# Optimization experiments

Measured on AMD Instinct MI355X. Metric: run time of the kernel, lower is better.

Reference implementation:

```python
import jax, jax.numpy as jnp
import numpy as np

T, B, OBS, H, P, L, A = 512, 128, 512, 256, 128, 4, 4


def _ln(x, scale, bias, eps=1e-6):
    mu = jnp.mean(x, axis=-1, keepdims=True)
    var = jnp.mean((x - mu) ** 2, axis=-1, keepdims=True)
    return (x - mu) * jax.lax.rsqrt(var + eps) * scale + bias


def _binop(qi, qj):
    # S5 reset-aware associative operator: elements (A, b, reset_flag)
    Ai, bi, ci = qi
    Aj, bj, cj = qj
    A = (Aj * Ai) * (1.0 - cj) + Aj * cj
    b = (Aj * bi + bj) * (1.0 - cj) + bj * cj
    c = ci * (1.0 - cj) + cj
    return A, b, c


def _s5_layer(x, dones, h0, scale, bias, lam_re, lam_im, b_re, b_im, c_re, c_im, d_vec, log_step, glu_W, glu_b):
    # x: (T,B,H) real, dones: (T,B), h0: (B,P) complex64
    skip = x
    u = _ln(x, scale, bias)                                  # prenorm
    lam = lam_re + 1j * lam_im                               # (P,)
    step = jnp.exp(log_step)                                 # (P,)
    lam_bar = jnp.exp(lam * step)                            # ZOH discretization
    B_bar = ((lam_bar - 1.0) / lam)[:, None] * (b_re + 1j * b_im)  # (P,H)
    Bu = jnp.einsum('tbh,ph->tbp', u.astype(jnp.complex64), B_bar)  # (T,B,P)
    A_el = jnp.concatenate([jnp.ones((1, B, P), jnp.complex64),
                            jnp.broadcast_to(lam_bar.astype(jnp.complex64), (T, B, P))], axis=0)
    b_el = jnp.concatenate([h0[None], Bu], axis=0)
    c_el = jnp.concatenate([jnp.zeros((1, B, 1), jnp.float32), dones[..., None]], axis=0)
    _, xs, _ = jax.lax.associative_scan(_binop, (A_el, b_el, c_el), axis=0)
    xs = xs[1:]                                              # (T,B,P) complex states
    new_h = xs[-1]
    C = c_re + 1j * c_im                                     # (H,P)
    ys = 2.0 * jnp.real(jnp.einsum('tbp,hp->tbh', xs, C)) + d_vec * u  # conj_sym output + D*u
    z = _ln(ys, scale, bias)                                 # gtrxl norm (shared LayerNorm params)
    z = jax.nn.gelu(z)                                       # half_glu1
    z = z * jax.nn.sigmoid(z @ glu_W + glu_b)
    return skip + z, new_h


def setup_inputs() -> dict:
    key = jax.random.key(0)
    ks = jax.random.split(key, 40)
    f32 = jnp.float32

    def n(i, shape, s=1.0):
        return jax.random.normal(ks[i], shape, f32) * s

    inp = {}
    inp['obs'] = n(0, (T, B, OBS))
    inp['dones'] = (jax.random.uniform(ks[1], (T, B)) < 0.01).astype(f32)
    inp['hidden_re'] = jnp.zeros((L, B, P), f32)
    inp['hidden_im'] = jnp.zeros((L, B, P), f32)
    inp['enc0_W'] = n(2, (OBS, 128), 1.0 / np.sqrt(OBS))
    inp['enc0_b'] = jnp.zeros((128,), f32)
    inp['enc1_W'] = n(3, (128, H), 1.0 / np.sqrt(128))
    inp['enc1_b'] = jnp.zeros((H,), f32)
    inp['norm_scale'] = jnp.ones((L, H), f32)
    inp['norm_bias'] = jnp.zeros((L, H), f32)
    inp['Lambda_re'] = -0.5 * jax.random.uniform(ks[4], (L, P), f32) - 0.1
    inp['Lambda_im'] = n(5, (L, P), np.pi)
    inp['B_re'] = n(6, (L, P, H), 1.0 / np.sqrt(H))
    inp['B_im'] = n(7, (L, P, H), 1.0 / np.sqrt(H))
    inp['C_re'] = n(8, (L, H, P), 1.0 / np.sqrt(2 * P))
    inp['C_im'] = n(9, (L, H, P), 1.0 / np.sqrt(2 * P))
    inp['D'] = n(10, (L, H))
    inp['log_step'] = jax.random.uniform(ks[11], (L, P), f32, np.log(1e-3), np.log(1e-1))
    inp['glu_W'] = n(12, (L, H, H), 1.0 / np.sqrt(H))
    inp['glu_b'] = jnp.zeros((L, H), f32)
    inp['ab0_W'] = n(13, (H, 128), 1.0 / np.sqrt(H))
    inp['ab0_b'] = jnp.zeros((128,), f32)
    inp['ab1_W'] = n(14, (128, 128), 1.0 / np.sqrt(128))
    inp['ab1_b'] = jnp.zeros((128,), f32)
    inp['adec_W'] = n(15, (128, A), 0.01 / np.sqrt(128))
    inp['adec_b'] = jnp.full((A,), 0.5, f32)
    inp['log_std'] = jnp.full((A,), -0.7, f32)
    inp['vb0_W'] = n(16, (H, 128), 1.0 / np.sqrt(H))
    inp['vb0_b'] = jnp.zeros((128,), f32)
    inp['vb1_W'] = n(17, (128, 128), 1.0 / np.sqrt(128))
    inp['vb1_b'] = jnp.zeros((128,), f32)
    inp['vdec_W'] = n(18, (128, 1), 1.0 / np.sqrt(128))
    inp['vdec_b'] = jnp.zeros((1,), f32)
    return inp


def reference(obs, dones, hidden_re, hidden_im, enc0_W, enc0_b, enc1_W, enc1_b,
              norm_scale, norm_bias, Lambda_re, Lambda_im, B_re, B_im, C_re, C_im,
              D, log_step, glu_W, glu_b, ab0_W, ab0_b, ab1_W, ab1_b, adec_W, adec_b,
              log_std, vb0_W, vb0_b, vb1_W, vb1_b, vdec_W, vdec_b):
    e = jax.nn.leaky_relu(obs @ enc0_W + enc0_b)
    e = jax.nn.leaky_relu(e @ enc1_W + enc1_b)
    h0 = (hidden_re + 1j * hidden_im).astype(jnp.complex64)  # (L,B,P)
    new_h = []
    for l in range(L):
        e, hl = _s5_layer(e, dones, h0[l], norm_scale[l], norm_bias[l],
                          Lambda_re[l], Lambda_im[l], B_re[l], B_im[l],
                          C_re[l], C_im[l], D[l], log_step[l], glu_W[l], glu_b[l])
        new_h.append(hl)
    new_h = jnp.stack(new_h)
    am = jax.nn.leaky_relu(e @ ab0_W + ab0_b)
    am = jax.nn.leaky_relu(am @ ab1_W + ab1_b)
    am = am @ adec_W + adec_b                                # actor mean (T,B,A)
    v = jax.nn.leaky_relu(e @ vb0_W + vb0_b)
    v = jax.nn.leaky_relu(v @ vb1_W + vb1_b)
    v = v @ vdec_W + vdec_b                                  # critic (T,B,1)
    sc = jnp.broadcast_to(jnp.exp(log_std), am.shape)        # Normal scale (pi params)
    out = jnp.concatenate([am, sc, v], axis=-1)              # (T,B,2A+1)
    return out, jnp.real(new_h), jnp.imag(new_h)
```

## Files before the change

kernel.cpp:

```cpp
#include <hip/hip_runtime.h>
#include <math.h>

#define TT 512
#define BB 128
#define OBSD 512
#define HD 256
#define PD 128
#define LD 4
#define NTB (TT*BB)

typedef __bf16 bf16x8 __attribute__((ext_vector_type(8)));
typedef float  f32x4  __attribute__((ext_vector_type(4)));

__device__ __forceinline__ float bf2f(unsigned short u) {
    return __uint_as_float(((unsigned)u) << 16);
}
__device__ __forceinline__ unsigned short f2bf(float f) {
    unsigned u = __float_as_uint(f);
    unsigned r = (u + 0x7FFFu + ((u >> 16) & 1u)) >> 16;
    return (unsigned short)r;
}
__device__ __forceinline__ float gelu_f(float x) {
    float x3 = x * x * x;
    return 0.5f * x * (1.f + tanhf(0.7978845608028654f * (x + 0.044715f * x3)));
}

template<int MODE, int NJ>
__global__ __launch_bounds__(256) void mgemm2(
    const unsigned short* __restrict__ A, const unsigned short* __restrict__ BT,
    int K, const float* __restrict__ bias,
    const float* __restrict__ lnsc, const float* __restrict__ lnbi,
    const unsigned short* __restrict__ aux1, unsigned short* Xio,
    unsigned short* __restrict__ U, int wU)
{
    const int N = NJ * 64;
    __shared__ unsigned short smA[64 * 32];
    __shared__ unsigned short smB[NJ * 64 * 32];
    __shared__ float2 red[64][4];
    int tid = threadIdx.x;
    int lane = tid & 63, w = tid >> 6;
    int m16 = lane & 15, quad = lane >> 4;
    int m0 = blockIdx.x * 64;

    f32x4 acc[4][NJ] = {};

    for (int k0 = 0; k0 < K; k0 += 32) {
        {
            const unsigned short* g = A + (size_t)(m0 + (tid >> 2)) * K + k0 + (tid & 3) * 8;
            unsigned short* l = smA + tid * 8;
            __builtin_amdgcn_global_load_lds(
                (const __attribute__((address_space(1))) void*)g,
                (__attribute__((address_space(3))) void*)l, 16, 0, 0);
        }
#pragma unroll
        for (int p = 0; p < NJ; ++p) {
            const unsigned short* g = BT + (size_t)(p * 64 + (tid >> 2)) * K + k0 + (tid & 3) * 8;
            unsigned short* l = smB + p * 2048 + tid * 8;
            __builtin_amdgcn_global_load_lds(
                (const __attribute__((address_space(1))) void*)g,
                (__attribute__((address_space(3))) void*)l, 16, 0, 0);
        }
        __syncthreads();
        bf16x8 af[4], bfr[NJ];
#pragma unroll
        for (int mi = 0; mi < 4; ++mi)
            af[mi] = *(const bf16x8*)(smA + (mi * 16 + m16) * 32 + quad * 8);
#pragma unroll
        for (int nj = 0; nj < NJ; ++nj)
            bfr[nj] = *(const bf16x8*)(smB + (w * NJ * 16 + nj * 16 + m16) * 32 + quad * 8);
#pragma unroll
        for (int mi = 0; mi < 4; ++mi)
#pragma unroll
            for (int nj = 0; nj < NJ; ++nj)
                acc[mi][nj] = __builtin_amdgcn_mfma_f32_16x16x32_bf16(
                    bfr[nj], af[mi], acc[mi][nj], 0, 0, 0);
        __syncthreads();
    }

    int colb = w * NJ * 16 + quad * 4;

    if (MODE == 1) {
#pragma unroll
        for (int mi = 0; mi < 4; ++mi) {
            size_t rowb = (size_t)(m0 + mi * 16 + m16) * N;
#pragma unroll
            for (int nj = 0; nj < NJ; ++nj) {
                ushort4 o = { f2bf(acc[mi][nj][0]), f2bf(acc[mi][nj][1]),
                              f2bf(acc[mi][nj][2]), f2bf(acc[mi][nj][3]) };
                *(ushort4*)(U + rowb + colb + nj * 16) = o;
            }
        }
        return;
    }

    float4 bn[NJ];
#pragma unroll
    for (int nj = 0; nj < NJ; ++nj) bn[nj] = *(const float4*)(bias + colb + nj * 16);

#pragma unroll
    for (int mi = 0; mi < 4; ++mi) {
        size_t rowb = (size_t)(m0 + mi * 16 + m16) * N;
        float s = 0.f, q = 0.f;
#pragma unroll
        for (int nj = 0; nj < NJ; ++nj) {
            ushort4 a1, xo;
            if (MODE == 2 || MODE == 3) a1 = *(const ushort4*)(aux1 + rowb + colb + nj * 16);
            if (MODE == 3)              xo = *(const ushort4*)(Xio + rowb + colb + nj * 16);
            float vv[4];
#pragma unroll
            for (int r = 0; r < 4; ++r) {
                float v = acc[mi][nj][r];
                float bv = (r == 0) ? bn[nj].x : (r == 1) ? bn[nj].y : (r == 2) ? bn[nj].z : bn[nj].w;
                if (MODE == 0 || MODE == 4) {
                    v += bv; v = v > 0.f ? v : 0.01f * v;
                } else if (MODE == 2) {
                    float u = bf2f(r == 0 ? a1.x : r == 1 ? a1.y : r == 2 ? a1.z : a1.w);
                    v += bv * u;
                } else if (MODE == 3) {
                    float zz = bf2f(r == 0 ? a1.x : r == 1 ? a1.y : r == 2 ? a1.z : a1.w);
                    float xx = bf2f(r == 0 ? xo.x : r == 1 ? xo.y : r == 2 ? xo.z : xo.w);
                    float sg = 1.f / (1.f + expf(-(v + bv)));
                    v = xx + zz * sg;
                }
                vv[r] = v;
                acc[mi][nj][r] = v;
                s += v; q += v * v;
            }
            if (MODE == 0 || MODE == 3) {
                ushort4 o = { f2bf(vv[0]), f2bf(vv[1]), f2bf(vv[2]), f2bf(vv[3]) };
                *(ushort4*)(Xio + rowb + colb + nj * 16) = o;
            } else if (MODE == 4) {
                ushort4 o = { f2bf(vv[0]), f2bf(vv[1]), f2bf(vv[2]), f2bf(vv[3]) };
                *(ushort4*)(U + rowb + colb + nj * 16) = o;
            }
        }
        if (MODE != 4 && (MODE != 3 || wU)) {
            s += __shfl_xor(s, 16); q += __shfl_xor(q, 16);
            s += __shfl_xor(s, 32); q += __shfl_xor(q, 32);
            if (quad == 0) red[mi * 16 + m16][w] = float2{s, q};
        }
    }
    if (MODE == 4 || (MODE == 3 && !wU)) return;
    __syncthreads();

    float4 ls[NJ], lb[NJ];
#pragma unroll
    for (int nj = 0; nj < NJ; ++nj) {
        ls[nj] = *(const float4*)(lnsc + colb + nj * 16);
        lb[nj] = *(const float4*)(lnbi + colb + nj * 16);
    }
#pragma unroll
    for (int mi = 0; mi < 4; ++mi) {
        int row_l = mi * 16 + m16;
        float2 t0 = red[row_l][0], t1 = red[row_l][1], t2 = red[row_l][2], t3 = red[row_l][3];
        float S = t0.x + t1.x + t2.x + t3.x;
        float Q = t0.y + t1.y + t2.y + t3.y;
        float mu = S * (1.f / 256.f);
        float var = Q * (1.f / 256.f) - mu * mu;
        float rstd = rsqrtf(var + 1e-6f);
        size_t rowb = (size_t)(m0 + row_l) * N;
#pragma unroll
        for (int nj = 0; nj < NJ; ++nj) {
            float o[4];
#pragma unroll
            for (int r = 0; r < 4; ++r) {
                float sc = (r == 0) ? ls[nj].x : (r == 1) ? ls[nj].y : (r == 2) ? ls[nj].z : ls[nj].w;
                float bi = (r == 0) ? lb[nj].x : (r == 1) ? lb[nj].y : (r == 2) ? lb[nj].z : lb[nj].w;
                float v = (acc[mi][nj][r] - mu) * rstd * sc + bi;
                if (MODE == 2) v = gelu_f(v);
                o[r] = v;
            }
            ushort4 ov = { f2bf(o[0]), f2bf(o[1]), f2bf(o[2]), f2bf(o[3]) };
            *(ushort4*)(U + rowb + colb + nj * 16) = ov;
        }
    }
}

__global__ __launch_bounds__(256) void mgemm_obs(
    const float* __restrict__ A, const unsigned short* __restrict__ BT,
    unsigned short* __restrict__ U, const float* __restrict__ bias)
{
    const int K = 512, NJ = 2, N = 128;
    __shared__ unsigned short smA[64 * 32];
    __shared__ unsigned short smB[NJ * 64 * 32];
    int tid = threadIdx.x;
    int lane = tid & 63, w = tid >> 6;
    int m16 = lane & 15, quad = lane >> 4;
    int m0 = blockIdx.x * 64;

    f32x4 acc[4][NJ] = {};
    for (int k0 = 0; k0 < K; k0 += 32) {
#pragma unroll
        for (int p = 0; p < 2; ++p) {
            int idx = p * 256 + tid;
            int r = idx >> 3, kq = (idx & 7) * 4;
            float4 v = *(const float4*)(A + (size_t)(m0 + r) * K + k0 + kq);
            ushort4 o = { f2bf(v.x), f2bf(v.y), f2bf(v.z), f2bf(v.w) };
            *(ushort4*)(smA + r * 32 + kq) = o;
        }
#pragma unroll
        for (int p = 0; p < NJ; ++p) {
            const unsigned short* g = BT + (size_t)(p * 64 + (tid >> 2)) * K + k0 + (tid & 3) * 8;
            unsigned short* l = smB + p * 2048 + tid * 8;
            __builtin_amdgcn_global_load_lds(
                (const __attribute__((address_space(1))) void*)g,
                (__attribute__((address_space(3))) void*)l, 16, 0, 0);
        }
        __syncthreads();
        bf16x8 af[4], bfr[NJ];
#pragma unroll
        for (int mi = 0; mi < 4; ++mi)
            af[mi] = *(const bf16x8*)(smA + (mi * 16 + m16) * 32 + quad * 8);
#pragma unroll
        for (int nj = 0; nj < NJ; ++nj)
            bfr[nj] = *(const bf16x8*)(smB + (w * NJ * 16 + nj * 16 + m16) * 32 + quad * 8);
#pragma unroll
        for (int mi = 0; mi < 4; ++mi)
#pragma unroll
            for (int nj = 0; nj < NJ; ++nj)
                acc[mi][nj] = __builtin_amdgcn_mfma_f32_16x16x32_bf16(
                    bfr[nj], af[mi], acc[mi][nj], 0, 0, 0);
        __syncthreads();
    }
    int colb = w * NJ * 16 + quad * 4;
#pragma unroll
    for (int mi = 0; mi < 4; ++mi) {
        size_t rowb = (size_t)(m0 + mi * 16 + m16) * N;
#pragma unroll
        for (int nj = 0; nj < NJ; ++nj) {
            float4 bv = *(const float4*)(bias + colb + nj * 16);
            float v0 = acc[mi][nj][0] + bv.x; v0 = v0 > 0.f ? v0 : 0.01f * v0;
            float v1 = acc[mi][nj][1] + bv.y; v1 = v1 > 0.f ? v1 : 0.01f * v1;
            float v2 = acc[mi][nj][2] + bv.z; v2 = v2 > 0.f ? v2 : 0.01f * v2;
            float v3 = acc[mi][nj][3] + bv.w; v3 = v3 > 0.f ? v3 : 0.01f * v3;
            ushort4 o = { f2bf(v0), f2bf(v1), f2bf(v2), f2bf(v3) };
            *(ushort4*)(U + rowb + colb + nj * 16) = o;
        }
    }
}

__global__ __launch_bounds__(512) void scan2_k(
    const unsigned short* __restrict__ bu, unsigned short* __restrict__ xs,
    const float* __restrict__ dones,
    const float* __restrict__ h0re, const float* __restrict__ h0im,
    const float* __restrict__ lamre, const float* __restrict__ lamim,
    const float* __restrict__ lstep,
    float* __restrict__ outre, float* __restrict__ outim)
{
    __shared__ float sdone[TT];
    __shared__ float4 ssum[8][64];
    __shared__ float2 shin[8][64];
    int tid = threadIdx.x;
    int b  = blockIdx.x >> 1;
    int ph = blockIdx.x & 1;
    int chunk = tid >> 6, pl = tid & 63;
    int p = ph * 64 + pl;
    sdone[tid] = dones[tid * BB + b];
    float lr = lamre[p], li = lamim[p];
    float st = expf(lstep[p]);
    float er = expf(lr * st);
    float ar = er * cosf(li * st);
    float ai = er * sinf(li * st);
    __syncthreads();

    int t0 = chunk * 64;
    unsigned buf[64];
    float Ar = 1.f, Ai = 0.f, br = 0.f, bi = 0.f;
#pragma unroll
    for (int j = 0; j < 64; ++j) {
        size_t off = ((size_t)(t0 + j) * BB + b) * 256 + 2 * p;
        unsigned v = *(const unsigned*)(bu + off);
        buf[j] = v;
        float bur = bf2f((unsigned short)(v & 0xFFFFu));
        float bui = bf2f((unsigned short)(v >> 16));
        if (sdone[t0 + j] != 0.f) {
            Ar = 0.f; Ai = 0.f; br = bur; bi = bui;
        } else {
            float nAr = ar * Ar - ai * Ai;
            float nAi = ar * Ai + ai * Ar;
            float nbr = fmaf(ar, br, fmaf(-ai, bi, bur));
            float nbi = fmaf(ar, bi, fmaf(ai, br, bui));
            Ar = nAr; Ai = nAi; br = nbr; bi = nbi;
        }
    }
    ssum[chunk][pl] = float4{Ar, Ai, br, bi};
    __syncthreads();
    if (tid < 64) {
        int gid = b * 128 + p;
        float hr = h0re[gid], hi = h0im[gid];
#pragma unroll
        for (int c = 0; c < 8; ++c) {
            shin[c][pl] = float2{hr, hi};
            float4 s = ssum[c][pl];
            float nhr = fmaf(s.x, hr, fmaf(-s.y, hi, s.z));
            float nhi = fmaf(s.x, hi, fmaf(s.y, hr, s.w));
            hr = nhr; hi = nhi;
        }
        outre[gid] = hr; outim[gid] = hi;
    }
    __syncthreads();
    float hr = shin[chunk][pl].x, hi = shin[chunk][pl].y;
#pragma unroll
    for (int j = 0; j < 64; ++j) {
        unsigned v = buf[j];
        float bur = bf2f((unsigned short)(v & 0xFFFFu));
        float bui = bf2f((unsigned short)(v >> 16));
        float nr, ni;
        if (sdone[t0 + j] != 0.f) { nr = bur; ni = bui; }
        else {
            nr = fmaf(ar, hr, fmaf(-ai, hi, bur));
            ni = fmaf(ar, hi, fmaf(ai, hr, bui));
        }
        hr = nr; hi = ni;
        size_t off = ((size_t)(t0 + j) * BB + b) * 256 + 2 * p;
        *(unsigned*)(xs + off) = ((unsigned)f2bf(ni) << 16) | f2bf(nr);
    }
}

__global__ __launch_bounds__(256) void prep_k(
    const float* __restrict__ Br, const float* __restrict__ Bi,
    const float* __restrict__ Cr, const float* __restrict__ Ci,
    const float* __restrict__ Lr, const float* __restrict__ Li,
    const float* __restrict__ ls, unsigned short* bbarT, unsigned short* ccatT)
{
    int gid = blockIdx.x * 256 + threadIdx.x;
    int l = gid >> 15;
    int rem = gid & 32767;
    int p = rem >> 8;
    int h = rem & 255;
    float lr = Lr[l * PD + p], li = Li[l * PD + p];
    float st = expf(ls[l * PD + p]);
    float er = expf(lr * st);
    float lbr = er * cosf(li * st);
    float lbi = er * sinf(li * st);
    float nr = lbr - 1.f, ni = lbi;
    float den = lr * lr + li * li;
    float fr = (nr * lr + ni * li) / den;
    float fi = (ni * lr - nr * li) / den;
    float bre = Br[(size_t)(l * PD + p) * HD + h];
    float bim = Bi[(size_t)(l * PD + p) * HD + h];
    size_t lb = (size_t)l * 65536;
    bbarT[lb + (size_t)(2 * p) * 256 + h]     = f2bf(fr * bre - fi * bim);
    bbarT[lb + (size_t)(2 * p + 1) * 256 + h] = f2bf(fr * bim + fi * bre);
    float cre = Cr[(size_t)(l * HD + h) * PD + p];
    float cim = Ci[(size_t)(l * HD + h) * PD + p];
    ccatT[lb + (size_t)h * 256 + 2 * p]     = f2bf(2.f * cre);
    ccatT[lb + (size_t)h * 256 + 2 * p + 1] = f2bf(-2.f * cim);
}

__global__ __launch_bounds__(256) void tcvt_k(const float* __restrict__ in,
    unsigned short* __restrict__ out, int K, int N)
{
    int gid = blockIdx.x * 256 + threadIdx.x;
    if (gid >= K * N) return;
    int k = gid / N, n = gid - k * N;
    out[(size_t)n * K + k] = f2bf(in[gid]);
}

__global__ __launch_bounds__(256) void head_k(
    const unsigned short* __restrict__ am2, const unsigned short* __restrict__ v2,
    const float* __restrict__ adW, const float* __restrict__ adb,
    const float* __restrict__ lstd,
    const float* __restrict__ vdW, const float* __restrict__ vdb,
    float* out)
{
    int wid = threadIdx.x >> 6, lane = threadIdx.x & 63;
    size_t row = (size_t)blockIdx.x * 4 + wid;
    float a1 = bf2f(am2[row * 128 + lane]);
    float a2 = bf2f(am2[row * 128 + 64 + lane]);
    float w1 = bf2f(v2[row * 128 + lane]);
    float w2 = bf2f(v2[row * 128 + 64 + lane]);
    float vals[5];
#pragma unroll
    for (int a = 0; a < 4; ++a)
        vals[a] = a1 * adW[lane * 4 + a] + a2 * adW[(lane + 64) * 4 + a];
    vals[4] = w1 * vdW[lane] + w2 * vdW[64 + lane];
#pragma unroll
    for (int off = 32; off; off >>= 1)
#pragma unroll
        for (int k = 0; k < 5; ++k) vals[k] += __shfl_xor(vals[k], off);
    if (lane == 0) {
        size_t o = row * 9;
#pragma unroll
        for (int a = 0; a < 4; ++a) out[o + a] = vals[a] + adb[a];
#pragma unroll
        for (int a = 0; a < 4; ++a) out[o + 4 + a] = expf(lstd[a]);
        out[o + 8] = vals[4] + vdb[0];
    }
}

extern "C" void kernel_launch(void* const* d_in, const int* in_sizes, int n_in,
                              void* d_out, int out_size, void* d_ws, size_t ws_size,
                              hipStream_t stream) {
    (void)in_sizes; (void)n_in; (void)out_size; (void)ws_size;
    const float* obs     = (const float*)d_in[0];
    const float* dones   = (const float*)d_in[1];
    const float* hre     = (const float*)d_in[2];
    const float* him     = (const float*)d_in[3];
    const float* enc0_W  = (const float*)d_in[4];
    const float* enc0_b  = (const float*)d_in[5];
    const float* enc1_W  = (const float*)d_in[6];
    const float* enc1_b  = (const float*)d_in[7];
    const float* nsc     = (const float*)d_in[8];
    const float* nbi     = (const float*)d_in[9];
    const float* Lre     = (const float*)d_in[10];
    const float* Lim     = (const float*)d_in[11];
    const float* B_re    = (const float*)d_in[12];
    const float* B_im    = (const float*)d_in[13];
    const float* C_re    = (const float*)d_in[14];
    const float* C_im    = (const float*)d_in[15];
    const float* Dv      = (const float*)d_in[16];
    const float* lstep   = (const float*)d_in[17];
    const float* glu_W   = (const float*)d_in[18];
    const float* glu_b   = (const float*)d_in[19];
    const float* ab0_W   = (const float*)d_in[20];
    const float* ab0_b   = (const float*)d_in[21];
    const float* ab1_W   = (const float*)d_in[22];
    const float* ab1_b   = (const float*)d_in[23];
    const float* adec_W  = (const float*)d_in[24];
    const float* adec_b  = (const float*)d_in[25];
    const float* log_std = (const float*)d_in[26];
    const float* vb0_W   = (const float*)d_in[27];
    const float* vb0_b   = (const float*)d_in[28];
    const float* vb1_W   = (const float*)d_in[29];
    const float* vb1_b   = (const float*)d_in[30];
    const float* vdec_W  = (const float*)d_in[31];
    const float* vdec_b  = (const float*)d_in[32];

    const size_t MB = (size_t)1 << 20;
    char* wsb = (char*)d_ws;
    unsigned short* XS    = (unsigned short*)(wsb);
    unsigned short* AM1   = (unsigned short*)(wsb);
    unsigned short* V1    = (unsigned short*)(wsb + 16 * MB);
    unsigned short* AM2   = (unsigned short*)(wsb + 32 * MB);
    unsigned short* V2    = (unsigned short*)(wsb + 48 * MB);
    unsigned short* U1    = (unsigned short*)(wsb + 64 * MB);
    unsigned short* X     = (unsigned short*)(wsb + 96 * MB);
    unsigned short* U     = (unsigned short*)(wsb + 128 * MB);
    unsigned short* BU    = (unsigned short*)(wsb + 160 * MB);
    char* wgt = wsb + 192 * MB;
    unsigned short* BBART = (unsigned short*)(wgt);
    unsigned short* CCATT = (unsigned short*)(wgt + 512 * 1024);
    unsigned short* GLUT  = (unsigned short*)(wgt + 1024 * 1024);
    unsigned short* E0T   = (unsigned short*)(wgt + 1536 * 1024);
    unsigned short* E1T   = (unsigned short*)(wgt + 1664 * 1024);
    unsigned short* AB0T  = (unsigned short*)(wgt + 1728 * 1024);
    unsigned short* AB1T  = (unsigned short*)(wgt + 1792 * 1024);
    unsigned short* VB0T  = (unsigned short*)(wgt + 1824 * 1024);
    unsigned short* VB1T  = (unsigned short*)(wgt + 1888 * 1024);

    float* out   = (float*)d_out;
    float* outre = out + (size_t)NTB * 9;
    float* outim = outre + LD * BB * PD;

    prep_k<<<512, 256, 0, stream>>>(B_re, B_im, C_re, C_im, Lre, Lim, lstep, BBART, CCATT);
    tcvt_k<<<256, 256, 0, stream>>>(enc0_W, E0T, 512, 128);
    tcvt_k<<<128, 256, 0, stream>>>(enc1_W, E1T, 128, 256);
    for (int l = 0; l < LD; ++l)
        tcvt_k<<<256, 256, 0, stream>>>(glu_W + (size_t)l * 65536, GLUT + (size_t)l * 65536, 256, 256);
    tcvt_k<<<128, 256, 0, stream>>>(ab0_W, AB0T, 256, 128);
    tcvt_k<<<64, 256, 0, stream>>>(ab1_W, AB1T, 128, 128);
    tcvt_k<<<128, 256, 0, stream>>>(vb0_W, VB0T, 256, 128);
    tcvt_k<<<64, 256, 0, stream>>>(vb1_W, VB1T, 128, 128);

    mgemm_obs<<<1024, 256, 0, stream>>>(obs, E0T, U1, enc0_b);
    mgemm2<0, 4><<<1024, 256, 0, stream>>>(U1, E1T, 128, enc1_b, nsc, nbi, nullptr, X, U, 1);

    for (int l = 0; l < LD; ++l) {
        mgemm2<1, 4><<<1024, 256, 0, stream>>>(U, BBART + (size_t)l * 65536, 256,
                                               nullptr, nullptr, nullptr, nullptr, nullptr, BU, 0);
        scan2_k<<<256, 512, 0, stream>>>(BU, XS, dones, hre + l * BB * PD, him + l * BB * PD,
                                         Lre + l * PD, Lim + l * PD, lstep + l * PD,
                                         outre + l * BB * PD, outim + l * BB * PD);
        mgemm2<2, 4><<<1024, 256, 0, stream>>>(XS, CCATT + (size_t)l * 65536, 256,
                                               Dv + l * HD, nsc + l * HD, nbi + l * HD, U, nullptr, U, 1);
        const float* nsc2 = nsc + ((l + 1 < LD) ? (l + 1) * HD : 0);
        const float* nbi2 = nbi + ((l + 1 < LD) ? (l + 1) * HD : 0);
        mgemm2<3, 4><<<1024, 256, 0, stream>>>(U, GLUT + (size_t)l * 65536, 256,
                                               glu_b + l * HD, nsc2, nbi2, U, X, U, (l + 1 < LD) ? 1 : 0);
    }

    mgemm2<4, 2><<<1024, 256, 0, stream>>>(X, AB0T, 256, ab0_b, nullptr, nullptr, nullptr, nullptr, AM1, 0);
    mgemm2<4, 2><<<1024, 256, 0, stream>>>(AM1, AB1T, 128, ab1_b, nullptr, nullptr, nullptr, nullptr, AM2, 0);
    mgemm2<4, 2><<<1024, 256, 0, stream>>>(X, VB0T, 256, vb0_b, nullptr, nullptr, nullptr, nullptr, V1, 0);
    mgemm2<4, 2><<<1024, 256, 0, stream>>>(V1, VB1T, 128, vb1_b, nullptr, nullptr, nullptr, nullptr, V2, 0);
    head_k<<<NTB / 4, 256, 0, stream>>>(AM2, V2, adec_W, adec_b, log_std, vdec_W, vdec_b, out);
}
```

Before: 988.0 us.

## Fuse C-projection, GLU and next-layer B-projection into one per-layer kernel

Adds a mega kernel that runs the C-projection GEMM with D-skip, LayerNorm and GELU, then the GLU GEMM with sigmoid gating and residual, then the next LayerNorm and the next layer's B-projection GEMM. The 64-row activation tile stays in LDS between the three GEMMs, replacing three separate launches per layer. This is meant to remove global-memory round trips of the intermediate activations and cut launch count. The first layer's B-projection is hoisted before the loop, and the four GLU weight transposes become a single launch. In exchange each block needs more LDS and runs three GEMMs back to back, which may lower occupancy and add serial latency.

```diff
diff --git a/kernel.cpp b/kernel.cpp
--- a/kernel.cpp
+++ b/kernel.cpp
@@ -11,6 +11,7 @@
 
 typedef __bf16 bf16x8 __attribute__((ext_vector_type(8)));
 typedef float  f32x4  __attribute__((ext_vector_type(4)));
+typedef unsigned short u16x8 __attribute__((ext_vector_type(8)));
 
 __device__ __forceinline__ float bf2f(unsigned short u) {
     return __uint_as_float(((unsigned)u) << 16);
@@ -103,30 +104,17 @@
         float s = 0.f, q = 0.f;
 #pragma unroll
         for (int nj = 0; nj < NJ; ++nj) {
-            ushort4 a1, xo;
-            if (MODE == 2 || MODE == 3) a1 = *(const ushort4*)(aux1 + rowb + colb + nj * 16);
-            if (MODE == 3)              xo = *(const ushort4*)(Xio + rowb + colb + nj * 16);
             float vv[4];
 #pragma unroll
             for (int r = 0; r < 4; ++r) {
                 float v = acc[mi][nj][r];
                 float bv = (r == 0) ? bn[nj].x : (r == 1) ? bn[nj].y : (r == 2) ? bn[nj].z : bn[nj].w;
-                if (MODE == 0 || MODE == 4) {
-                    v += bv; v = v > 0.f ? v : 0.01f * v;
-                } else if (MODE == 2) {
-                    float u = bf2f(r == 0 ? a1.x : r == 1 ? a1.y : r == 2 ? a1.z : a1.w);
-                    v += bv * u;
-                } else if (MODE == 3) {
-                    float zz = bf2f(r == 0 ? a1.x : r == 1 ? a1.y : r == 2 ? a1.z : a1.w);
-                    float xx = bf2f(r == 0 ? xo.x : r == 1 ? xo.y : r == 2 ? xo.z : xo.w);
-                    float sg = 1.f / (1.f + expf(-(v + bv)));
-                    v = xx + zz * sg;
-                }
+                v += bv; v = v > 0.f ? v : 0.01f * v;
                 vv[r] = v;
                 acc[mi][nj][r] = v;
                 s += v; q += v * v;
             }
-            if (MODE == 0 || MODE == 3) {
+            if (MODE == 0) {
                 ushort4 o = { f2bf(vv[0]), f2bf(vv[1]), f2bf(vv[2]), f2bf(vv[3]) };
                 *(ushort4*)(Xio + rowb + colb + nj * 16) = o;
             } else if (MODE == 4) {
@@ -134,13 +122,13 @@
                 *(ushort4*)(U + rowb + colb + nj * 16) = o;
             }
         }
-        if (MODE != 4 && (MODE != 3 || wU)) {
+        if (MODE != 4) {
             s += __shfl_xor(s, 16); q += __shfl_xor(q, 16);
             s += __shfl_xor(s, 32); q += __shfl_xor(q, 32);
             if (quad == 0) red[mi * 16 + m16][w] = float2{s, q};
         }
     }
-    if (MODE == 4 || (MODE == 3 && !wU)) return;
+    if (MODE == 4) return;
     __syncthreads();
 
     float4 ls[NJ], lb[NJ];
@@ -167,11 +155,231 @@
                 float sc = (r == 0) ? ls[nj].x : (r == 1) ? ls[nj].y : (r == 2) ? ls[nj].z : ls[nj].w;
                 float bi = (r == 0) ? lb[nj].x : (r == 1) ? lb[nj].y : (r == 2) ? lb[nj].z : lb[nj].w;
                 float v = (acc[mi][nj][r] - mu) * rstd * sc + bi;
-                if (MODE == 2) v = gelu_f(v);
                 o[r] = v;
             }
             ushort4 ov = { f2bf(o[0]), f2bf(o[1]), f2bf(o[2]), f2bf(o[3]) };
             *(ushort4*)(U + rowb + colb + nj * 16) = ov;
+        }
+    }
+}
+
+#define ZSTRIDE 264
+__device__ __forceinline__ void kloop256(
+    const unsigned short* __restrict__ Bp,
+    const unsigned short* zbuf, unsigned short* smB,
+    int tid, int w, int m16, int quad, f32x4 acc[4][4])
+{
+    for (int k0 = 0; k0 < 256; k0 += 32) {
+#pragma unroll
+        for (int p = 0; p < 4; ++p) {
+            const unsigned short* g = Bp + (size_t)((p * 64 + (tid >> 2)) * 256 + k0 + (tid & 3) * 8);
+            unsigned short* l = smB + p * 2048 + tid * 8;
+            __builtin_amdgcn_global_load_lds(
+                (const __attribute__((address_space(1))) void*)g,
+                (__attribute__((address_space(3))) void*)l, 16, 0, 0);
+        }
+        __syncthreads();
+        bf16x8 af[4], bfr[4];
+#pragma unroll
+        for (int mi = 0; mi < 4; ++mi)
+            af[mi] = *(const bf16x8*)(zbuf + (mi * 16 + m16) * ZSTRIDE + k0 + quad * 8);
+#pragma unroll
+        for (int nj = 0; nj < 4; ++nj)
+            bfr[nj] = *(const bf16x8*)(smB + (w * 64 + nj * 16 + m16) * 32 + quad * 8);
+#pragma unroll
+        for (int mi = 0; mi < 4; ++mi)
+#pragma unroll
+            for (int nj = 0; nj < 4; ++nj)
+                acc[mi][nj] = __builtin_amdgcn_mfma_f32_16x16x32_bf16(
+                    bfr[nj], af[mi], acc[mi][nj], 0, 0, 0);
+        __syncthreads();
+    }
+}
+
+template<int LAST>
+__global__ __launch_bounds__(256) void mega_k(
+    const unsigned short* __restrict__ XSp,
+    const unsigned short* __restrict__ Uaux,
+    unsigned short* __restrict__ Xio,
+    const unsigned short* __restrict__ CT,
+    const unsigned short* __restrict__ GT,
+    const unsigned short* __restrict__ BT2,
+    const float* __restrict__ Dv,
+    const float* __restrict__ ns1, const float* __restrict__ nb1,
+    const float* __restrict__ glub,
+    const float* __restrict__ ns2, const float* __restrict__ nb2,
+    unsigned short* __restrict__ Uo,
+    unsigned short* __restrict__ BUo)
+{
+    const int N = 256;
+    __shared__ unsigned short zbuf[64 * ZSTRIDE];
+    __shared__ unsigned short smB[4 * 2048];
+    __shared__ float2 red[64][4];
+    int tid = threadIdx.x;
+    int lane = tid & 63, w = tid >> 6;
+    int m16 = lane & 15, quad = lane >> 4;
+    int m0 = blockIdx.x * 64;
+    int colb = w * 64 + quad * 4;
+
+#pragma unroll
+    for (int i = 0; i < 8; ++i) {
+        int c = i * 256 + tid;
+        int r = c >> 5, cc = (c & 31) * 8;
+        u16x8 v = *(const u16x8*)(XSp + (size_t)(m0 + r) * N + cc);
+        *(u16x8*)(zbuf + r * ZSTRIDE + cc) = v;
+    }
+
+    f32x4 acc[4][4] = {};
+    kloop256(CT, zbuf, smB, tid, w, m16, quad, acc);
+
+    float4 dn[4];
+#pragma unroll
+    for (int nj = 0; nj < 4; ++nj) dn[nj] = *(const float4*)(Dv + colb + nj * 16);
+#pragma unroll
+    for (int mi = 0; mi < 4; ++mi) {
+        size_t rowb = (size_t)(m0 + mi * 16 + m16) * N;
+        float s = 0.f, q = 0.f;
+#pragma unroll
+        for (int nj = 0; nj < 4; ++nj) {
+            ushort4 a1 = *(const ushort4*)(Uaux + rowb + colb + nj * 16);
+#pragma unroll
+            for (int r = 0; r < 4; ++r) {
+                float d = (r == 0) ? dn[nj].x : (r == 1) ? dn[nj].y : (r == 2) ? dn[nj].z : dn[nj].w;
+                float u = bf2f(r == 0 ? a1.x : r == 1 ? a1.y : r == 2 ? a1.z : a1.w);
+                float v = acc[mi][nj][r] + d * u;
+                acc[mi][nj][r] = v;
+                s += v; q += v * v;
+            }
+        }
+        s += __shfl_xor(s, 16); q += __shfl_xor(q, 16);
+        s += __shfl_xor(s, 32); q += __shfl_xor(q, 32);
+        if (quad == 0) red[mi * 16 + m16][w] = float2{s, q};
+    }
+    __syncthreads();
+    {
+        float4 ls[4], lb[4];
+#pragma unroll
+        for (int nj = 0; nj < 4; ++nj) {
+            ls[nj] = *(const float4*)(ns1 + colb + nj * 16);
+            lb[nj] = *(const float4*)(nb1 + colb + nj * 16);
+        }
+#pragma unroll
+        for (int mi = 0; mi < 4; ++mi) {
+            int row_l = mi * 16 + m16;
+            float2 t0 = red[row_l][0], t1 = red[row_l][1], t2 = red[row_l][2], t3 = red[row_l][3];
+            float S = t0.x + t1.x + t2.x + t3.x;
+            float Q = t0.y + t1.y + t2.y + t3.y;
+            float mu = S * (1.f / 256.f);
+            float var = Q * (1.f / 256.f) - mu * mu;
+            float rstd = rsqrtf(var + 1e-6f);
+#pragma unroll
+            for (int nj = 0; nj < 4; ++nj) {
+                float o[4];
+#pragma unroll
+                for (int r = 0; r < 4; ++r) {
+                    float sc = (r == 0) ? ls[nj].x : (r == 1) ? ls[nj].y : (r == 2) ? ls[nj].z : ls[nj].w;
+                    float bi = (r == 0) ? lb[nj].x : (r == 1) ? lb[nj].y : (r == 2) ? lb[nj].z : lb[nj].w;
+                    o[r] = gelu_f((acc[mi][nj][r] - mu) * rstd * sc + bi);
+                }
+                ushort4 ov = { f2bf(o[0]), f2bf(o[1]), f2bf(o[2]), f2bf(o[3]) };
+                *(ushort4*)(zbuf + row_l * ZSTRIDE + colb + nj * 16) = ov;
+            }
+        }
+    }
+
+#pragma unroll
+    for (int mi = 0; mi < 4; ++mi)
+#pragma unroll
+        for (int nj = 0; nj < 4; ++nj)
+#pragma unroll
+            for (int r = 0; r < 4; ++r) acc[mi][nj][r] = 0.f;
+    kloop256(GT, zbuf, smB, tid, w, m16, quad, acc);
+
+    float4 gb[4];
+#pragma unroll
+    for (int nj = 0; nj < 4; ++nj) gb[nj] = *(const float4*)(glub + colb + nj * 16);
+#pragma unroll
+    for (int mi = 0; mi < 4; ++mi) {
+        int row_l = mi * 16 + m16;
+        size_t rowb = (size_t)(m0 + row_l) * N;
+        float s = 0.f, q = 0.f;
+#pragma unroll
+        for (int nj = 0; nj < 4; ++nj) {
+            ushort4 zz = *(const ushort4*)(zbuf + row_l * ZSTRIDE + colb + nj * 16);
+            ushort4 xx = *(const ushort4*)(Xio + rowb + colb + nj * 16);
+            float o[4];
+#pragma unroll
+            for (int r = 0; r < 4; ++r) {
+                float g = (r == 0) ? gb[nj].x : (r == 1) ? gb[nj].y : (r == 2) ? gb[nj].z : gb[nj].w;
+                float zv = bf2f(r == 0 ? zz.x : r == 1 ? zz.y : r == 2 ? zz.z : zz.w);
+                float xv = bf2f(r == 0 ? xx.x : r == 1 ? xx.y : r == 2 ? xx.z : xx.w);
+                float sg = 1.f / (1.f + expf(-(acc[mi][nj][r] + g)));
+                float v = xv + zv * sg;
+                o[r] = v;
+                acc[mi][nj][r] = v;
+                s += v; q += v * v;
+            }
+            ushort4 ov = { f2bf(o[0]), f2bf(o[1]), f2bf(o[2]), f2bf(o[3]) };
+            *(ushort4*)(Xio + rowb + colb + nj * 16) = ov;
+        }
+        if (!LAST) {
+            s += __shfl_xor(s, 16); q += __shfl_xor(q, 16);
+            s += __shfl_xor(s, 32); q += __shfl_xor(q, 32);
+            if (quad == 0) red[mi * 16 + m16][w] = float2{s, q};
+        }
+    }
+    if (LAST) return;
+    __syncthreads();
+
+    {
+        float4 ls[4], lb[4];
+#pragma unroll
+        for (int nj = 0; nj < 4; ++nj) {
+            ls[nj] = *(const float4*)(ns2 + colb + nj * 16);
+            lb[nj] = *(const float4*)(nb2 + colb + nj * 16);
+        }
+#pragma unroll
+        for (int mi = 0; mi < 4; ++mi) {
+            int row_l = mi * 16 + m16;
+            float2 t0 = red[row_l][0], t1 = red[row_l][1], t2 = red[row_l][2], t3 = red[row_l][3];
+            float S = t0.x + t1.x + t2.x + t3.x;
+            float Q = t0.y + t1.y + t2.y + t3.y;
+            float mu = S * (1.f / 256.f);
+            float var = Q * (1.f / 256.f) - mu * mu;
+            float rstd = rsqrtf(var + 1e-6f);
+            size_t rowb = (size_t)(m0 + row_l) * N;
+#pragma unroll
+            for (int nj = 0; nj < 4; ++nj) {
+                float o[4];
+#pragma unroll
+                for (int r = 0; r < 4; ++r) {
+                    float sc = (r == 0) ? ls[nj].x : (r == 1) ? ls[nj].y : (r == 2) ? ls[nj].z : ls[nj].w;
+                    float bi = (r == 0) ? lb[nj].x : (r == 1) ? lb[nj].y : (r == 2) ? lb[nj].z : lb[nj].w;
+                    o[r] = (acc[mi][nj][r] - mu) * rstd * sc + bi;
+                }
+                ushort4 ov = { f2bf(o[0]), f2bf(o[1]), f2bf(o[2]), f2bf(o[3]) };
+                *(ushort4*)(zbuf + row_l * ZSTRIDE + colb + nj * 16) = ov;
+                *(ushort4*)(Uo + rowb + colb + nj * 16) = ov;
+            }
+        }
+    }
+
+#pragma unroll
+    for (int mi = 0; mi < 4; ++mi)
+#pragma unroll
+        for (int nj = 0; nj < 4; ++nj)
+#pragma unroll
+            for (int r = 0; r < 4; ++r) acc[mi][nj][r] = 0.f;
+    kloop256(BT2, zbuf, smB, tid, w, m16, quad, acc);
+
+#pragma unroll
+    for (int mi = 0; mi < 4; ++mi) {
+        size_t rowb = (size_t)(m0 + mi * 16 + m16) * N;
+#pragma unroll
+        for (int nj = 0; nj < 4; ++nj) {
+            ushort4 o = { f2bf(acc[mi][nj][0]), f2bf(acc[mi][nj][1]),
+                          f2bf(acc[mi][nj][2]), f2bf(acc[mi][nj][3]) };
+            *(ushort4*)(BUo + rowb + colb + nj * 16) = o;
         }
     }
 }
@@ -355,6 +563,16 @@
     if (gid >= K * N) return;
     int k = gid / N, n = gid - k * N;
     out[(size_t)n * K + k] = f2bf(in[gid]);
+}
+
+__global__ __launch_bounds__(256) void tcvt4_k(const float* __restrict__ in,
+    unsigned short* __restrict__ out)
+{
+    int gid = blockIdx.x * 256 + threadIdx.x;
+    int l = gid >> 16;
+    int rem = gid & 65535;
+    int k = rem >> 8, n = rem & 255;
+    out[(size_t)l * 65536 + (size_t)n * 256 + k] = f2bf(in[gid]);
 }
 
 __global__ __launch_bounds__(256) void head_k(
@@ -456,8 +674,7 @@
     prep_k<<<512, 256, 0, stream>>>(B_re, B_im, C_re, C_im, Lre, Lim, lstep, BBART, CCATT);
     tcvt_k<<<256, 256, 0, stream>>>(enc0_W, E0T, 512, 128);
     tcvt_k<<<128, 256, 0, stream>>>(enc1_W, E1T, 128, 256);
-    for (int l = 0; l < LD; ++l)
-        tcvt_k<<<256, 256, 0, stream>>>(glu_W + (size_t)l * 65536, GLUT + (size_t)l * 65536, 256, 256);
+    tcvt4_k<<<1024, 256, 0, stream>>>(glu_W, GLUT);
     tcvt_k<<<128, 256, 0, stream>>>(ab0_W, AB0T, 256, 128);
     tcvt_k<<<64, 256, 0, stream>>>(ab1_W, AB1T, 128, 128);
     tcvt_k<<<128, 256, 0, stream>>>(vb0_W, VB0T, 256, 128);
@@ -466,18 +683,23 @@
     mgemm_obs<<<1024, 256, 0, stream>>>(obs, E0T, U1, enc0_b);
     mgemm2<0, 4><<<1024, 256, 0, stream>>>(U1, E1T, 128, enc1_b, nsc, nbi, nullptr, X, U, 1);
 
+    mgemm2<1, 4><<<1024, 256, 0, stream>>>(U, BBART, 256,
+                                           nullptr, nullptr, nullptr, nullptr, nullptr, BU, 0);
     for (int l = 0; l < LD; ++l) {
-        mgemm2<1, 4><<<1024, 256, 0, stream>>>(U, BBART + (size_t)l * 65536, 256,
-                                               nullptr, nullptr, nullptr, nullptr, nullptr, BU, 0);
         scan2_k<<<256, 512, 0, stream>>>(BU, XS, dones, hre + l * BB * PD, him + l * BB * PD,
                                          Lre + l * PD, Lim + l * PD, lstep + l * PD,
                                          outre + l * BB * PD, outim + l * BB * PD);
-        mgemm2<2, 4><<<1024, 256, 0, stream>>>(XS, CCATT + (size_t)l * 65536, 256,
-                                               Dv + l * HD, nsc + l * HD, nbi + l * HD, U, nullptr, U, 1);
-        const float* nsc2 = nsc + ((l + 1 < LD) ? (l + 1) * HD : 0);
-        const float* nbi2 = nbi + ((l + 1 < LD) ? (l + 1) * HD : 0);
-        mgemm2<3, 4><<<1024, 256, 0, stream>>>(U, GLUT + (size_t)l * 65536, 256,
-                                               glu_b + l * HD, nsc2, nbi2, U, X, U, (l + 1 < LD) ? 1 : 0);
+        if (l + 1 < LD)
+            mega_k<0><<<1024, 256, 0, stream>>>(XS, U, X,
+                CCATT + (size_t)l * 65536, GLUT + (size_t)l * 65536,
+                BBART + (size_t)(l + 1) * 65536,
+                Dv + l * HD, nsc + l * HD, nbi + l * HD, glu_b + l * HD,
+                nsc + (l + 1) * HD, nbi + (l + 1) * HD, U, BU);
+        else
+            mega_k<1><<<1024, 256, 0, stream>>>(XS, U, X,
+                CCATT + (size_t)l * 65536, GLUT + (size_t)l * 65536, nullptr,
+                Dv + l * HD, nsc + l * HD, nbi + l * HD, glu_b + l * HD,
+                nullptr, nullptr, nullptr, nullptr);
     }
 
     mgemm2<4, 2><<<1024, 256, 0, stream>>>(X, AB0T, 256, ab0_b, nullptr, nullptr, nullptr, nullptr, AM1, 0);
```

Result: slower. 1.077 ms (+9.0%).

## Double-buffer LDS tiles in mgemm2 and batch GLU weight conversion

Applied to the files above, without the earlier changes.

The GEMM main loop now uses two LDS buffers, so the async global-to-LDS loads for the next K tile are issued before the current tile's MFMAs run. A partial vmcnt wait and raw s_barrier replace the full syncthreads. The reduction scratch array is aliased onto smA to keep LDS usage down. Separately, the four per-layer GLU weight transpose launches are merged into one kernel to cut launch overhead.

```diff
diff --git a/kernel.cpp b/kernel.cpp
--- a/kernel.cpp
+++ b/kernel.cpp
@@ -34,9 +34,9 @@
     unsigned short* __restrict__ U, int wU)
 {
     const int N = NJ * 64;
-    __shared__ unsigned short smA[64 * 32];
-    __shared__ unsigned short smB[NJ * 64 * 32];
-    __shared__ float2 red[64][4];
+    __shared__ unsigned short smA[2][64 * 32];
+    __shared__ unsigned short smB[2][NJ * 64 * 32];
+    float2 (*red)[4] = reinterpret_cast<float2(*)[4]>(&smA[0][0]);
     int tid = threadIdx.x;
     int lane = tid & 63, w = tid >> 6;
     int m16 = lane & 15, quad = lane >> 4;
@@ -44,37 +44,47 @@
 
     f32x4 acc[4][NJ] = {};
 
-    for (int k0 = 0; k0 < K; k0 += 32) {
-        {
-            const unsigned short* g = A + (size_t)(m0 + (tid >> 2)) * K + k0 + (tid & 3) * 8;
-            unsigned short* l = smA + tid * 8;
+    auto stage = [&](int bu, int k0) {
+        const unsigned short* g = A + (size_t)(m0 + (tid >> 2)) * K + k0 + (tid & 3) * 8;
+        __builtin_amdgcn_global_load_lds(
+            (const __attribute__((address_space(1))) void*)g,
+            (__attribute__((address_space(3))) void*)(&smA[bu][0] + tid * 8), 16, 0, 0);
+#pragma unroll
+        for (int p = 0; p < NJ; ++p) {
+            const unsigned short* gb = BT + (size_t)(p * 64 + (tid >> 2)) * K + k0 + (tid & 3) * 8;
             __builtin_amdgcn_global_load_lds(
-                (const __attribute__((address_space(1))) void*)g,
-                (__attribute__((address_space(3))) void*)l, 16, 0, 0);
-        }
-#pragma unroll
-        for (int p = 0; p < NJ; ++p) {
-            const unsigned short* g = BT + (size_t)(p * 64 + (tid >> 2)) * K + k0 + (tid & 3) * 8;
-            unsigned short* l = smB + p * 2048 + tid * 8;
-            __builtin_amdgcn_global_load_lds(
-                (const __attribute__((address_space(1))) void*)g,
-                (__attribute__((address_space(3))) void*)l, 16, 0, 0);
-        }
-        __syncthreads();
+                (const __attribute__((address_space(1))) void*)gb,
+                (__attribute__((address_space(3))) void*)(&smB[bu][0] + p * 2048 + tid * 8), 16, 0, 0);
+        }
+    };
+
+    int nk = K >> 5;
+    stage(0, 0);
+    for (int t = 0; t < nk; ++t) {
+        int cur = t & 1;
+        if (t + 1 < nk) {
+            stage(cur ^ 1, (t + 1) << 5);
+            asm volatile("s_waitcnt vmcnt(%0)" :: "i"(NJ + 1) : "memory");
+        } else {
+            asm volatile("s_waitcnt vmcnt(0)" ::: "memory");
+        }
+        __builtin_amdgcn_s_barrier();
+        __builtin_amdgcn_sched_barrier(0);
         bf16x8 af[4], bfr[NJ];
 #pragma unroll
         for (int mi = 0; mi < 4; ++mi)
-            af[mi] = *(const bf16x8*)(smA + (mi * 16 + m16) * 32 + quad * 8);
+            af[mi] = *(const bf16x8*)(&smA[cur][0] + (mi * 16 + m16) * 32 + quad * 8);
 #pragma unroll
         for (int nj = 0; nj < NJ; ++nj)
-            bfr[nj] = *(const bf16x8*)(smB + (w * NJ * 16 + nj * 16 + m16) * 32 + quad * 8);
+            bfr[nj] = *(const bf16x8*)(&smB[cur][0] + (w * NJ * 16 + nj * 16 + m16) * 32 + quad * 8);
 #pragma unroll
         for (int mi = 0; mi < 4; ++mi)
 #pragma unroll
             for (int nj = 0; nj < NJ; ++nj)
                 acc[mi][nj] = __builtin_amdgcn_mfma_f32_16x16x32_bf16(
                     bfr[nj], af[mi], acc[mi][nj], 0, 0, 0);
-        __syncthreads();
+        __builtin_amdgcn_sched_barrier(0);
+        __builtin_amdgcn_s_barrier();
     }
 
     int colb = w * NJ * 16 + quad * 4;
@@ -355,6 +365,16 @@
     if (gid >= K * N) return;
     int k = gid / N, n = gid - k * N;
     out[(size_t)n * K + k] = f2bf(in[gid]);
+}
+
+__global__ __launch_bounds__(256) void tcvt4_k(const float* __restrict__ in,
+    unsigned short* __restrict__ out)
+{
+    int gid = blockIdx.x * 256 + threadIdx.x;
+    int l = gid >> 16;
+    int rem = gid & 65535;
+    int k = rem >> 8, n = rem & 255;
+    out[(size_t)l * 65536 + (size_t)n * 256 + k] = f2bf(in[gid]);
 }
 
 __global__ __launch_bounds__(256) void head_k(
@@ -456,8 +476,7 @@
     prep_k<<<512, 256, 0, stream>>>(B_re, B_im, C_re, C_im, Lre, Lim, lstep, BBART, CCATT);
     tcvt_k<<<256, 256, 0, stream>>>(enc0_W, E0T, 512, 128);
     tcvt_k<<<128, 256, 0, stream>>>(enc1_W, E1T, 128, 256);
-    for (int l = 0; l < LD; ++l)
-        tcvt_k<<<256, 256, 0, stream>>>(glu_W + (size_t)l * 65536, GLUT + (size_t)l * 65536, 256, 256);
+    tcvt4_k<<<1024, 256, 0, stream>>>(glu_W, GLUT);
     tcvt_k<<<128, 256, 0, stream>>>(ab0_W, AB0T, 256, 128);
     tcvt_k<<<64, 256, 0, stream>>>(ab1_W, AB1T, 128, 128);
     tcvt_k<<<128, 256, 0, stream>>>(vb0_W, VB0T, 256, 128);
```

Result: faster. 964.5 us (-2.4%).
